# Performance work log

Hardware: AMD Instinct MI355X
Metric: run time of the kernel (lower is better)

Reference implementation:

```python
import jax, jax.numpy as jnp
import numpy as np


def _ln(x, g, eps=1e-5):
    # channel LayerNorm over dim 1, unbiased=False variance
    mean = jnp.mean(x, axis=1, keepdims=True)
    var = jnp.mean((x - mean) ** 2, axis=1, keepdims=True)
    return (x - mean) * jax.lax.rsqrt(var + eps) * g


def _c11(x, w, b):
    # 1x1 conv: w (O,C), b (O,)
    return jnp.einsum('bchw,oc->bohw', x, w) + b[None, :, None, None]


def _dw(x, w, b):
    # depthwise 3x3 conv, SAME padding; w (C,1,3,3), b (C,)
    C = x.shape[1]
    y = jax.lax.conv_general_dilated(x, w, (1, 1), 'SAME',
                                     feature_group_count=C,
                                     dimension_numbers=('NCHW', 'OIHW', 'NCHW'))
    return y + b[None, :, None, None]


def _forward(F_i, F_w, g1, g2, qw1, qb1, kw1, kb1, vw1, vb1,
             qw2, qb2, kw2, kb2, vw2, vb2,
             qdw1, qdb1, kdw1, kdb1, vdw1, vdb1,
             qdw2, qdb2, kdw2, kdb2, vdw2, vdb2, lw, lb):
    B, C1, H, W = F_i.shape
    C2 = F_w.shape[1]
    HW = H * W
    fi = _ln(F_i, g1)
    fw = _ln(F_w, g2)
    # qkv = 1x1 conv -> depthwise conv; then RAW C-order reshape (torch .view)
    Qi = _dw(_c11(fi, qw1, qb1), qdw1, qdb1).reshape(B, HW, C1)
    Ki = _dw(_c11(fi, kw1, kb1), kdw1, kdb1).reshape(B, HW, C1)
    Vi = _dw(_c11(fi, vw1, vb1), vdw1, vdb1).reshape(B, C1, HW)
    Qw = _dw(_c11(fw, qw2, qb2), qdw2, qdb2).reshape(B, HW, C2)
    Kw = _dw(_c11(fw, kw2, kb2), kdw2, kdb2).reshape(B, HW, C2)
    Vw = _dw(_c11(fw, vw2, vb2), vdw2, vdb2).reshape(B, C2, HW)
    # channel cross-attention: (B,C1,HW)@(B,HW,C2) -> (B,C1,C2)
    a1 = jax.nn.softmax(jnp.einsum('bnc,bnd->bcd', Qi, Kw), axis=-1)
    a2 = jax.nn.softmax(jnp.einsum('bnc,bnd->bcd', Qw, Ki), axis=-1)
    Aw = jnp.einsum('bcd,bdn->bcn', a1, Vw).reshape(B, H, W, C2).transpose(0, 3, 1, 2)
    Ai = jnp.einsum('bcd,bdn->bcn', a2, Vi).reshape(B, H, W, C1).transpose(0, 3, 1, 2)
    cat = jnp.concatenate([Aw, Ai], axis=1)  # (B, C2+C1, H, W)
    Ct = cat.shape[1]
    flat = cat.reshape(B, Ct, HW).transpose(0, 2, 1).reshape(-1, Ct)  # (B*HW, Ct)
    out = flat @ lw.T + lb  # (B*HW, Cout)
    Cout = lb.shape[0]
    # faithful replication of torch's view/permute/view tail
    out = out.reshape(B, Cout, H, W).transpose(0, 2, 3, 1).reshape(B, Cout, H, W)
    return out + F_i + F_w


def setup_inputs() -> dict:
    key = jax.random.key(0)
    ks = jax.random.split(key, 20)
    B, C, H, W = 8, 128, 128, 128
    d = {}
    d['F_i'] = jax.random.normal(ks[0], (B, C, H, W), jnp.float32)
    d['F_w'] = jax.random.normal(ks[1], (B, C, H, W), jnp.float32)
    d['g1'] = jnp.ones((1, C, 1, 1), jnp.float32)
    d['g2'] = jnp.ones((1, C, 1, 1), jnp.float32)
    s = 1.0 / np.sqrt(C)
    i = 2
    for n in ['qw1', 'kw1', 'vw1', 'qw2', 'kw2', 'vw2']:
        d[n] = jax.random.normal(ks[i], (C, C), jnp.float32) * s
        i += 1
    for n in ['qb1', 'kb1', 'vb1', 'qb2', 'kb2', 'vb2']:
        d[n] = jnp.zeros((C,), jnp.float32)
    sd = 1.0 / 3.0
    for n in ['qdw1', 'kdw1', 'vdw1', 'qdw2', 'kdw2', 'vdw2']:
        d[n] = jax.random.normal(ks[i], (C, 1, 3, 3), jnp.float32) * sd
        i += 1
    for n in ['qdb1', 'kdb1', 'vdb1', 'qdb2', 'kdb2', 'vdb2']:
        d[n] = jnp.zeros((C,), jnp.float32)
    d['lw'] = jax.random.normal(ks[i], (C, 2 * C), jnp.float32) * (1.0 / np.sqrt(2 * C))
    d['lb'] = jnp.zeros((C,), jnp.float32)
    return d


def reference(F_i, F_w, g1, g2, qw1, qb1, kw1, kb1, vw1, vb1,
              qw2, qb2, kw2, kb2, vw2, vb2,
              qdw1, qdb1, kdw1, kdb1, vdw1, vdb1,
              qdw2, qdb2, kdw2, kdb2, vdw2, vdb2, lw, lb):
    return _forward(F_i, F_w, g1, g2, qw1, qb1, kw1, kb1, vw1, vb1,
                    qw2, qb2, kw2, kb2, vw2, vb2,
                    qdw1, qdb1, kdw1, kdb1, vdw1, vdb1,
                    qdw2, qdb2, kdw2, kdb2, vdw2, vdb2, lw, lb)
```

## Files before the change

### kernel.cpp

```cpp
#include <hip/hip_runtime.h>
#include <cstddef>
#include <cstring>

#define HW 16384
#define CC 128
#define NB 8
#define GB 4

typedef short bf16x8_t __attribute__((ext_vector_type(8)));
typedef float floatx4 __attribute__((ext_vector_type(4)));

__device__ inline unsigned short f2bf(float f) {
  unsigned u; __builtin_memcpy(&u, &f, 4);
  u += 0x7fffu + ((u >> 16) & 1u);
  return (unsigned short)(u >> 16);
}
__device__ inline float bf2f(unsigned short s) {
  unsigned u = ((unsigned)s) << 16; float f; __builtin_memcpy(&f, &u, 4);
  return f;
}

__global__ __launch_bounds__(256) void k_ln_stats(const float* __restrict__ x,
                                                  float* __restrict__ mean,
                                                  float* __restrict__ rstd) {
  int idx = blockIdx.x * 256 + threadIdx.x;
  int b = idx >> 14;
  int p = idx & (HW - 1);
  const float* xp = x + ((size_t)b << 21) + p;
  float s = 0.f, ss = 0.f;
  for (int c = 0; c < CC; ++c) {
    float v = xp[(size_t)c << 14];
    s += v;
    ss += v * v;
  }
  float m = s * (1.0f / CC);
  float var = ss * (1.0f / CC) - m * m;
  mean[idx] = m;
  rstd[idx] = rsqrtf(var + 1e-5f);
}

__global__ __launch_bounds__(256) void k_conv1x1_mfma(
    const float* __restrict__ X, const float* __restrict__ W,
    const float* __restrict__ bias, const float* __restrict__ g,
    const float* __restrict__ mean, const float* __restrict__ rstd,
    float* __restrict__ Y, int b0) {
  __shared__ __align__(16) float raw[32][132];
  __shared__ __align__(16) short Ah[128][40];
  __shared__ __align__(16) short Al[128][40];
  __shared__ __align__(16) short Bh[128][40];
  __shared__ __align__(16) short Bl[128][40];
  const int bl = blockIdx.y;
  const int b = b0 + bl;
  const int p0 = blockIdx.x * 128;
  const int t = threadIdx.x;
  const int lane = t & 63, wv = t >> 6;
  const int quad = lane >> 4, l15 = lane & 15;
  const int wr = wv >> 1, wc = wv & 1;

  const int s1c = t >> 3, s1p = (t & 7) * 16;
  const int sao = t >> 1, sas = (t & 1) * 16;
  const int s2p = t & 127, s2o = t >> 7;
  const float mu = mean[b * HW + p0 + s2p];
  const float rs = rstd[b * HW + p0 + s2p];

  const float* Xb = X + ((size_t)b << 21);
  floatx4 acc[4][4];
#pragma unroll
  for (int i = 0; i < 4; ++i)
#pragma unroll
    for (int j = 0; j < 4; ++j) acc[i][j] = (floatx4){0.f, 0.f, 0.f, 0.f};

  for (int k0 = 0; k0 < 128; k0 += 32) {
    {
      const float* xp = Xb + ((size_t)(k0 + s1c) << 14) + p0 + s1p;
#pragma unroll
      for (int u = 0; u < 4; ++u)
        *reinterpret_cast<float4*>(&raw[s1c][s1p + 4 * u]) =
            *reinterpret_cast<const float4*>(xp + 4 * u);
    }
    {
      const float* wp = W + sao * 128 + k0 + sas;
      const float* gp = g + k0 + sas;
      short th[16], tl[16];
#pragma unroll
      for (int j = 0; j < 16; ++j) {
        float v = wp[j] * gp[j];
        unsigned short h = f2bf(v);
        th[j] = (short)h;
        tl[j] = (short)f2bf(v - bf2f(h));
      }
#pragma unroll
      for (int j = 0; j < 2; ++j) {
        *reinterpret_cast<bf16x8_t*>(&Ah[sao][sas + 8 * j]) =
            *reinterpret_cast<bf16x8_t*>(&th[8 * j]);
        *reinterpret_cast<bf16x8_t*>(&Al[sao][sas + 8 * j]) =
            *reinterpret_cast<bf16x8_t*>(&tl[8 * j]);
      }
    }
    __syncthreads();
#pragma unroll
    for (int item = 0; item < 2; ++item) {
      const int oct = s2o + 2 * item;
      short th[8], tl[8];
#pragma unroll
      for (int jj = 0; jj < 8; ++jj) {
        float v = (raw[oct * 8 + jj][s2p] - mu) * rs;
        unsigned short h = f2bf(v);
        th[jj] = (short)h;
        tl[jj] = (short)f2bf(v - bf2f(h));
      }
      *reinterpret_cast<bf16x8_t*>(&Bh[s2p][oct * 8]) =
          *reinterpret_cast<bf16x8_t*>(&th[0]);
      *reinterpret_cast<bf16x8_t*>(&Bl[s2p][oct * 8]) =
          *reinterpret_cast<bf16x8_t*>(&tl[0]);
    }
    __syncthreads();
    bf16x8_t afh[4], afl[4], bfh[4], bfl[4];
#pragma unroll
    for (int i = 0; i < 4; ++i) {
      const int m = wr * 64 + i * 16 + l15;
      afh[i] = *reinterpret_cast<const bf16x8_t*>(&Ah[m][quad * 8]);
      afl[i] = *reinterpret_cast<const bf16x8_t*>(&Al[m][quad * 8]);
    }
#pragma unroll
    for (int j = 0; j < 4; ++j) {
      const int p = wc * 64 + j * 16 + l15;
      bfh[j] = *reinterpret_cast<const bf16x8_t*>(&Bh[p][quad * 8]);
      bfl[j] = *reinterpret_cast<const bf16x8_t*>(&Bl[p][quad * 8]);
    }
#pragma unroll
    for (int i = 0; i < 4; ++i)
#pragma unroll
      for (int j = 0; j < 4; ++j) {
        acc[i][j] = __builtin_amdgcn_mfma_f32_16x16x32_bf16(afh[i], bfh[j], acc[i][j], 0, 0, 0);
        acc[i][j] = __builtin_amdgcn_mfma_f32_16x16x32_bf16(afh[i], bfl[j], acc[i][j], 0, 0, 0);
        acc[i][j] = __builtin_amdgcn_mfma_f32_16x16x32_bf16(afl[i], bfh[j], acc[i][j], 0, 0, 0);
      }
    __syncthreads();
  }
  float* Yb = Y + ((size_t)bl << 21);
#pragma unroll
  for (int i = 0; i < 4; ++i) {
#pragma unroll
    for (int j = 0; j < 4; ++j) {
#pragma unroll
      for (int r = 0; r < 4; ++r) {
        const int o = wr * 64 + i * 16 + quad * 4 + r;
        const int p = p0 + wc * 64 + j * 16 + l15;
        Yb[((size_t)o << 14) + p] = acc[i][j][r] + bias[o];
      }
    }
  }
}

__global__ __launch_bounds__(256) void k_score_dw(
    const float* __restrict__ Yq, const float* __restrict__ Yk,
    const float* __restrict__ qdw, const float* __restrict__ qdb,
    const float* __restrict__ kdw, const float* __restrict__ kdb,
    float* __restrict__ P) {
  __shared__ __align__(16) float As[32][132];
  __shared__ __align__(16) float Bs[32][132];
  const int ch = blockIdx.x;
  const int bl = blockIdx.y;
  const int t = threadIdx.x;
  const int m0 = (t >> 4) * 8, n0 = (t & 15) * 8;
  const int h_loc = t >> 3;
  const int w0 = (t & 7) * 16;
  float acc[8][8];
#pragma unroll
  for (int i = 0; i < 8; ++i)
#pragma unroll
    for (int j = 0; j < 8; ++j) acc[i][j] = 0.f;
  const float* Yqb = Yq + ((size_t)bl << 21);
  const float* Ykb = Yk + ((size_t)bl << 21);
  const int cc = ch;

  for (int k0 = 0; k0 < 128; k0 += 32) {
    const int h = k0 + h_loc;
#pragma unroll
    for (int side = 0; side < 2; ++side) {
      const float* Yc = (side ? Ykb : Yqb) + ((size_t)cc << 14);
      const float* wt = (side ? kdw : qdw) + cc * 9;
      const float bias = (side ? kdb : qdb)[cc];
      float a[16];
#pragma unroll
      for (int j = 0; j < 16; ++j) a[j] = bias;
#pragma unroll
      for (int dy = 0; dy < 3; ++dy) {
        const int hh = h + dy - 1;
        if (hh < 0 || hh > 127) continue;
        const float* rp = Yc + (hh << 7) + w0;
        float4 f0 = *reinterpret_cast<const float4*>(rp);
        float4 f1 = *reinterpret_cast<const float4*>(rp + 4);
        float4 f2 = *reinterpret_cast<const float4*>(rp + 8);
        float4 f3 = *reinterpret_cast<const float4*>(rp + 12);
        float s[18];
        s[1] = f0.x;  s[2] = f0.y;  s[3] = f0.z;  s[4] = f0.w;
        s[5] = f1.x;  s[6] = f1.y;  s[7] = f1.z;  s[8] = f1.w;
        s[9] = f2.x;  s[10] = f2.y; s[11] = f2.z; s[12] = f2.w;
        s[13] = f3.x; s[14] = f3.y; s[15] = f3.z; s[16] = f3.w;
        s[0] = (w0 > 0) ? rp[-1] : 0.f;
        s[17] = (w0 < 112) ? rp[16] : 0.f;
        const float wa = wt[dy * 3 + 0], wb = wt[dy * 3 + 1], wc2 = wt[dy * 3 + 2];
#pragma unroll
        for (int j = 0; j < 16; ++j)
          a[j] = fmaf(s[j], wa, fmaf(s[j + 1], wb, fmaf(s[j + 2], wc2, a[j])));
      }
      float* dst = side ? &Bs[h_loc][w0] : &As[h_loc][w0];
#pragma unroll
      for (int j = 0; j < 16; ++j) dst[j] = a[j];
    }
    __syncthreads();
#pragma unroll
    for (int k = 0; k < 32; ++k) {
      const float4* ap = reinterpret_cast<const float4*>(&As[k][m0]);
      const float4* bp = reinterpret_cast<const float4*>(&Bs[k][n0]);
      float4 a0 = ap[0], a1 = ap[1];
      float4 b0v = bp[0], b1v = bp[1];
      float a[8] = {a0.x, a0.y, a0.z, a0.w, a1.x, a1.y, a1.z, a1.w};
      float bb[8] = {b0v.x, b0v.y, b0v.z, b0v.w, b1v.x, b1v.y, b1v.z, b1v.w};
#pragma unroll
      for (int i = 0; i < 8; ++i)
#pragma unroll
        for (int j = 0; j < 8; ++j) acc[i][j] = fmaf(a[i], bb[j], acc[i][j]);
    }
    __syncthreads();
  }
  float* Pp = P + ((size_t)(ch * GB + bl) << 14);
#pragma unroll
  for (int i = 0; i < 8; ++i)
#pragma unroll
    for (int j = 0; j < 8; ++j) Pp[(m0 + i) * 128 + n0 + j] = acc[i][j];
}

__global__ __launch_bounds__(256) void k_score_reduce(const float* __restrict__ P,
                                                      float* __restrict__ S) {
  int idx = blockIdx.x * 256 + threadIdx.x;
  int bl = idx >> 14;
  int rem = idx & 16383;
  float s = 0.f;
  for (int c = 0; c < 128; ++c) s += P[((size_t)(c * GB + bl) << 14) + rem];
  S[idx] = s;
}

__global__ __launch_bounds__(128) void k_softmax(float* __restrict__ S) {
  __shared__ float red[128];
  const int row = blockIdx.x;
  const int t = threadIdx.x;
  float v = S[row * 128 + t];
  red[t] = v;
  __syncthreads();
  for (int s = 64; s > 0; s >>= 1) {
    if (t < s) red[t] = fmaxf(red[t], red[t + s]);
    __syncthreads();
  }
  float mx = red[0];
  __syncthreads();
  float e = expf(v - mx);
  red[t] = e;
  __syncthreads();
  for (int s = 64; s > 0; s >>= 1) {
    if (t < s) red[t] += red[t + s];
    __syncthreads();
  }
  S[row * 128 + t] = e / red[0];
}

__global__ __launch_bounds__(256) void k_dw_t(const float* __restrict__ Y,
                                              const float* __restrict__ Kw,
                                              const float* __restrict__ db,
                                              unsigned short* __restrict__ Vt) {
  __shared__ unsigned short T[128][33];
  const int h = blockIdx.x;
  const int c0 = blockIdx.y * 32;
  const int bl = blockIdx.z;
  const int t = threadIdx.x;
  const int cl = t >> 3;
  const int w0 = (t & 7) * 16;
  const int c = c0 + cl;
  const float* Yc = Y + ((size_t)bl << 21) + ((size_t)c << 14);
  const float* wt = Kw + c * 9;
  float a[16];
#pragma unroll
  for (int j = 0; j < 16; ++j) a[j] = db[c];
#pragma unroll
  for (int dy = 0; dy < 3; ++dy) {
    const int hh = h + dy - 1;
    if (hh < 0 || hh > 127) continue;
    const float* rp = Yc + (hh << 7) + w0;
    float4 f0 = *reinterpret_cast<const float4*>(rp);
    float4 f1 = *reinterpret_cast<const float4*>(rp + 4);
    float4 f2 = *reinterpret_cast<const float4*>(rp + 8);
    float4 f3 = *reinterpret_cast<const float4*>(rp + 12);
    float s[18];
    s[1] = f0.x;  s[2] = f0.y;  s[3] = f0.z;  s[4] = f0.w;
    s[5] = f1.x;  s[6] = f1.y;  s[7] = f1.z;  s[8] = f1.w;
    s[9] = f2.x;  s[10] = f2.y; s[11] = f2.z; s[12] = f2.w;
    s[13] = f3.x; s[14] = f3.y; s[15] = f3.z; s[16] = f3.w;
    s[0] = (w0 > 0) ? rp[-1] : 0.f;
    s[17] = (w0 < 112) ? rp[16] : 0.f;
    const float wa = wt[dy * 3 + 0], wb = wt[dy * 3 + 1], wc2 = wt[dy * 3 + 2];
#pragma unroll
    for (int j = 0; j < 16; ++j)
      a[j] = fmaf(s[j], wa, fmaf(s[j + 1], wb, fmaf(s[j + 2], wc2, a[j])));
  }
#pragma unroll
  for (int j = 0; j < 16; ++j) T[w0 + j][cl] = f2bf(a[j]);
  __syncthreads();
  const int w = t >> 1, half = t & 1;
  unsigned short tmp[16];
#pragma unroll
  for (int j = 0; j < 16; ++j) tmp[j] = T[w][half * 16 + j];
  uint4 v0, v1;
  unsigned* vp0 = reinterpret_cast<unsigned*>(&v0);
  unsigned* vp1 = reinterpret_cast<unsigned*>(&v1);
#pragma unroll
  for (int j = 0; j < 4; ++j) {
    vp0[j] = (unsigned)tmp[2 * j] | ((unsigned)tmp[2 * j + 1] << 16);
    vp1[j] = (unsigned)tmp[8 + 2 * j] | ((unsigned)tmp[8 + 2 * j + 1] << 16);
  }
  unsigned short* dst = Vt + ((size_t)bl << 21) + ((size_t)((h << 7) + w) << 7)
                        + c0 + half * 16;
  *reinterpret_cast<uint4*>(dst) = v0;
  *reinterpret_cast<uint4*>(dst + 8) = v1;
}

__global__ __launch_bounds__(256) void k_av_mfma(
    const float* __restrict__ S, const unsigned short* __restrict__ Vt,
    unsigned short* __restrict__ O) {
  __shared__ __align__(16) short As[128][136];
  const int bl = blockIdx.y;
  const int p0 = blockIdx.x * 128;
  const int t = threadIdx.x;
  const int lane = t & 63, wv = t >> 6;
  const int quad = lane >> 4, l15 = lane & 15;
  const int wr = wv >> 1, wc = wv & 1;
  {
    const float* Ab = S + ((size_t)bl << 14);
    const int r = t >> 1, hf = (t & 1) * 64;
    const float* src = Ab + r * 128 + hf;
    short tmp[64];
#pragma unroll
    for (int j = 0; j < 64; ++j) tmp[j] = (short)f2bf(src[j]);
#pragma unroll
    for (int j = 0; j < 8; ++j)
      *reinterpret_cast<bf16x8_t*>(&As[r][hf + j * 8]) =
          *reinterpret_cast<bf16x8_t*>(&tmp[j * 8]);
  }
  __syncthreads();
  floatx4 acc[4][4];
#pragma unroll
  for (int i = 0; i < 4; ++i)
#pragma unroll
    for (int j = 0; j < 4; ++j) acc[i][j] = (floatx4){0.f, 0.f, 0.f, 0.f};
  const unsigned short* Vb = Vt + ((size_t)bl << 21);
#pragma unroll
  for (int d0 = 0; d0 < 128; d0 += 32) {
    bf16x8_t af[4], bf[4];
#pragma unroll
    for (int i = 0; i < 4; ++i) {
      const int m = wr * 64 + i * 16 + l15;
      af[i] = *reinterpret_cast<const bf16x8_t*>(&As[m][d0 + quad * 8]);
    }
#pragma unroll
    for (int j = 0; j < 4; ++j) {
      const int p = p0 + wc * 64 + j * 16 + l15;
      bf[j] = *reinterpret_cast<const bf16x8_t*>(Vb + ((size_t)p << 7) + d0 + quad * 8);
    }
#pragma unroll
    for (int i = 0; i < 4; ++i)
#pragma unroll
      for (int j = 0; j < 4; ++j)
        acc[i][j] = __builtin_amdgcn_mfma_f32_16x16x32_bf16(af[i], bf[j], acc[i][j], 0, 0, 0);
  }
  unsigned short* Ob = O + ((size_t)bl << 21);
#pragma unroll
  for (int i = 0; i < 4; ++i) {
#pragma unroll
    for (int j = 0; j < 4; ++j) {
#pragma unroll
      for (int r = 0; r < 4; ++r) {
        const int c = wr * 64 + i * 16 + quad * 4 + r;
        const int p = p0 + wc * 64 + j * 16 + l15;
        Ob[((size_t)c << 14) + p] = f2bf(acc[i][j][r]);
      }
    }
  }
}

__global__ __launch_bounds__(256) void k_final_mfma(
    const unsigned short* __restrict__ Abuf, const float* __restrict__ lw,
    const float* __restrict__ lb, const float* __restrict__ Fi,
    const float* __restrict__ Fw, float* __restrict__ out, int pass, int b0) {
  __shared__ __align__(16) short As[128][136];
  const int c2 = blockIdx.x;
  const int bl = blockIdx.y;
  const int b = b0 + bl;
  const int t = threadIdx.x;
  const int lane = t & 63, wv = t >> 6;
  const int quad = lane >> 4, l15 = lane & 15;
  const int wr = wv >> 1, wc = wv & 1;
  const int koff = pass * 128;
  {
    const int r = t >> 1, hf = (t & 1) * 64;
    const float* src = lw + r * 256 + koff + hf;
    short tmp[64];
#pragma unroll
    for (int j = 0; j < 64; ++j) tmp[j] = (short)f2bf(src[j]);
#pragma unroll
    for (int j = 0; j < 8; ++j)
      *reinterpret_cast<bf16x8_t*>(&As[r][hf + j * 8]) =
          *reinterpret_cast<bf16x8_t*>(&tmp[j * 8]);
  }
  __syncthreads();
  floatx4 acc[4][4];
#pragma unroll
  for (int i = 0; i < 4; ++i)
#pragma unroll
    for (int j = 0; j < 4; ++j) acc[i][j] = (floatx4){0.f, 0.f, 0.f, 0.f};
  const unsigned short* Ub = Abuf + ((size_t)bl << 21) + c2 * 128;
#pragma unroll
  for (int d0 = 0; d0 < 128; d0 += 32) {
    bf16x8_t af[4], bf[4];
#pragma unroll
    for (int i = 0; i < 4; ++i) {
      const int m = wr * 64 + i * 16 + l15;
      af[i] = *reinterpret_cast<const bf16x8_t*>(&As[m][d0 + quad * 8]);
    }
#pragma unroll
    for (int j = 0; j < 4; ++j) {
      const int n = wc * 64 + j * 16 + l15;
      bf[j] = *reinterpret_cast<const bf16x8_t*>(Ub + ((size_t)n << 14) + d0 + quad * 8);
    }
#pragma unroll
    for (int i = 0; i < 4; ++i)
#pragma unroll
      for (int j = 0; j < 4; ++j)
        acc[i][j] = __builtin_amdgcn_mfma_f32_16x16x32_bf16(af[i], bf[j], acc[i][j], 0, 0, 0);
  }
  const size_t obase = ((size_t)b << 21) + ((size_t)c2 << 14);
#pragma unroll
  for (int i = 0; i < 4; ++i) {
#pragma unroll
    for (int j = 0; j < 4; ++j) {
#pragma unroll
      for (int r = 0; r < 4; ++r) {
        const int h2 = wr * 64 + i * 16 + quad * 4 + r;
        const int w2 = wc * 64 + j * 16 + l15;
        const size_t a = obase + ((size_t)h2 << 7) + w2;
        if (pass == 0)
          out[a] = acc[i][j][r] + lb[h2] + Fi[a] + Fw[a];
        else
          out[a] += acc[i][j][r];
      }
    }
  }
}

extern "C" void kernel_launch(void* const* d_in, const int* in_sizes, int n_in,
                              void* d_out, int out_size, void* d_ws, size_t ws_size,
                              hipStream_t stream) {
  const float* F_i  = (const float*)d_in[0];
  const float* F_w  = (const float*)d_in[1];
  const float* g1   = (const float*)d_in[2];
  const float* g2   = (const float*)d_in[3];
  const float* qw1  = (const float*)d_in[4];
  const float* kw1  = (const float*)d_in[5];
  const float* vw1  = (const float*)d_in[6];
  const float* qw2  = (const float*)d_in[7];
  const float* kw2  = (const float*)d_in[8];
  const float* vw2  = (const float*)d_in[9];
  const float* qb1  = (const float*)d_in[10];
  const float* kb1  = (const float*)d_in[11];
  const float* vb1  = (const float*)d_in[12];
  const float* qb2  = (const float*)d_in[13];
  const float* kb2  = (const float*)d_in[14];
  const float* vb2  = (const float*)d_in[15];
  const float* qdw1 = (const float*)d_in[16];
  const float* kdw1 = (const float*)d_in[17];
  const float* vdw1 = (const float*)d_in[18];
  const float* qdw2 = (const float*)d_in[19];
  const float* kdw2 = (const float*)d_in[20];
  const float* vdw2 = (const float*)d_in[21];
  const float* qdb1 = (const float*)d_in[22];
  const float* kdb1 = (const float*)d_in[23];
  const float* vdb1 = (const float*)d_in[24];
  const float* qdb2 = (const float*)d_in[25];
  const float* kdb2 = (const float*)d_in[26];
  const float* vdb2 = (const float*)d_in[27];
  const float* lw   = (const float*)d_in[28];
  const float* lb   = (const float*)d_in[29];
  float* out = (float*)d_out;

  char* w = (char*)d_ws;
  const size_t NTOT = (size_t)NB * HW;
  float* meanI = (float*)w; w += NTOT * 4;
  float* rstdI = (float*)w; w += NTOT * 4;
  float* meanW = (float*)w; w += NTOT * 4;
  float* rstdW = (float*)w; w += NTOT * 4;
  float* S     = (float*)w; w += (size_t)GB * HW * 4;
  float* P     = (float*)w; w += (size_t)128 * GB * HW * 4;
  float* Yq    = (float*)w; w += ((size_t)GB << 21) * 4;
  char*  Ykreg = w;         w += ((size_t)GB << 21) * 4;
  float* Yk    = (float*)Ykreg;
  unsigned short* Vt   = (unsigned short*)Ykreg;
  unsigned short* Abuf = (unsigned short*)(Ykreg + ((size_t)GB << 21) * 2);

  dim3 blk(256);
  k_ln_stats<<<dim3(512), blk, 0, stream>>>(F_i, meanI, rstdI);
  k_ln_stats<<<dim3(512), blk, 0, stream>>>(F_w, meanW, rstdW);

  for (int b0 = 0; b0 < NB; b0 += GB) {
    k_conv1x1_mfma<<<dim3(128, GB), blk, 0, stream>>>(F_i, qw1, qb1, g1, meanI, rstdI, Yq, b0);
    k_conv1x1_mfma<<<dim3(128, GB), blk, 0, stream>>>(F_w, kw2, kb2, g2, meanW, rstdW, Yk, b0);
    k_score_dw<<<dim3(128, GB), blk, 0, stream>>>(Yq, Yk, qdw1, qdb1, kdw2, kdb2, P);
    k_score_reduce<<<dim3(GB * HW / 256), blk, 0, stream>>>(P, S);
    k_softmax<<<dim3(GB * 128), dim3(128), 0, stream>>>(S);
    k_conv1x1_mfma<<<dim3(128, GB), blk, 0, stream>>>(F_w, vw2, vb2, g2, meanW, rstdW, Yq, b0);
    k_dw_t<<<dim3(128, 4, GB), blk, 0, stream>>>(Yq, vdw2, vdb2, Vt);
    k_av_mfma<<<dim3(128, GB), blk, 0, stream>>>(S, Vt, Abuf);
    k_final_mfma<<<dim3(128, GB), blk, 0, stream>>>(Abuf, lw, lb, F_i, F_w, out, 0, b0);

    k_conv1x1_mfma<<<dim3(128, GB), blk, 0, stream>>>(F_w, qw2, qb2, g2, meanW, rstdW, Yq, b0);
    k_conv1x1_mfma<<<dim3(128, GB), blk, 0, stream>>>(F_i, kw1, kb1, g1, meanI, rstdI, Yk, b0);
    k_score_dw<<<dim3(128, GB), blk, 0, stream>>>(Yq, Yk, qdw2, qdb2, kdw1, kdb1, P);
    k_score_reduce<<<dim3(GB * HW / 256), blk, 0, stream>>>(P, S);
    k_softmax<<<dim3(GB * 128), dim3(128), 0, stream>>>(S);
    k_conv1x1_mfma<<<dim3(128, GB), blk, 0, stream>>>(F_i, vw1, vb1, g1, meanI, rstdI, Yq, b0);
    k_dw_t<<<dim3(128, 4, GB), blk, 0, stream>>>(Yq, vdw1, vdb1, Vt);
    k_av_mfma<<<dim3(128, GB), blk, 0, stream>>>(S, Vt, Abuf);
    k_final_mfma<<<dim3(128, GB), blk, 0, stream>>>(Abuf, lw, lb, F_i, F_w, out, 1, b0);
  }
}
```

Measured before the change: 922.0 us.

## Move score GEMM to split-bf16 MFMA and fuse both final projections

The per-channel score kernel now stages the depthwise-conv output in shared memory. It splits each value into a bf16 high and low pair and accumulates with three bf16 MFMAs per tile, replacing the scalar fp32 FMA outer product. Accuracy stays close to fp32 while the multiply work moves onto the matrix cores, at the cost of extra shared memory, extra syncs and conversion work. Separately, the two final-projection launches are merged into one kernel that reads both attention buffers. This removes the read-modify-write of the output and one extra pass over F_i and F_w. It needs a separate workspace buffer for A1.

```diff
diff --git a/kernel.cpp b/kernel.cpp
--- a/kernel.cpp
+++ b/kernel.cpp
@@ -153,35 +153,45 @@
   }
 }
 
-__global__ __launch_bounds__(256) void k_score_dw(
+__global__ __launch_bounds__(256) void k_score_mfma(
     const float* __restrict__ Yq, const float* __restrict__ Yk,
     const float* __restrict__ qdw, const float* __restrict__ qdb,
     const float* __restrict__ kdw, const float* __restrict__ kdb,
     float* __restrict__ P) {
-  __shared__ __align__(16) float As[32][132];
-  __shared__ __align__(16) float Bs[32][132];
+  __shared__ __align__(16) float raw[32][132];
+  __shared__ __align__(16) short Ah[128][40];
+  __shared__ __align__(16) short Al[128][40];
+  __shared__ __align__(16) short Bh[128][40];
+  __shared__ __align__(16) short Bl[128][40];
   const int ch = blockIdx.x;
   const int bl = blockIdx.y;
   const int t = threadIdx.x;
-  const int m0 = (t >> 4) * 8, n0 = (t & 15) * 8;
+  const int lane = t & 63, wv = t >> 6;
+  const int quad = lane >> 4, l15 = lane & 15;
+  const int wr = wv >> 1, wc = wv & 1;
   const int h_loc = t >> 3;
   const int w0 = (t & 7) * 16;
-  float acc[8][8];
-#pragma unroll
-  for (int i = 0; i < 8; ++i)
-#pragma unroll
-    for (int j = 0; j < 8; ++j) acc[i][j] = 0.f;
-  const float* Yqb = Yq + ((size_t)bl << 21);
-  const float* Ykb = Yk + ((size_t)bl << 21);
+  const int s2w = t & 127, s2o = t >> 7;
   const int cc = ch;
+  const float* Yqb = Yq + ((size_t)bl << 21) + ((size_t)cc << 14);
+  const float* Ykb = Yk + ((size_t)bl << 21) + ((size_t)cc << 14);
+  const float* qwt = qdw + cc * 9;
+  const float* kwt = kdw + cc * 9;
+  const float qbv = qdb[cc], kbv = kdb[cc];
+
+  floatx4 acc[4][4];
+#pragma unroll
+  for (int i = 0; i < 4; ++i)
+#pragma unroll
+    for (int j = 0; j < 4; ++j) acc[i][j] = (floatx4){0.f, 0.f, 0.f, 0.f};
 
   for (int k0 = 0; k0 < 128; k0 += 32) {
     const int h = k0 + h_loc;
 #pragma unroll
     for (int side = 0; side < 2; ++side) {
-      const float* Yc = (side ? Ykb : Yqb) + ((size_t)cc << 14);
-      const float* wt = (side ? kdw : qdw) + cc * 9;
-      const float bias = (side ? kdb : qdb)[cc];
+      const float* Yc = side ? Ykb : Yqb;
+      const float* wt = side ? kwt : qwt;
+      const float bias = side ? kbv : qbv;
       float a[16];
 #pragma unroll
       for (int j = 0; j < 16; ++j) a[j] = bias;
@@ -206,31 +216,66 @@
         for (int j = 0; j < 16; ++j)
           a[j] = fmaf(s[j], wa, fmaf(s[j + 1], wb, fmaf(s[j + 2], wc2, a[j])));
       }
-      float* dst = side ? &Bs[h_loc][w0] : &As[h_loc][w0];
-#pragma unroll
-      for (int j = 0; j < 16; ++j) dst[j] = a[j];
-    }
-    __syncthreads();
-#pragma unroll
-    for (int k = 0; k < 32; ++k) {
-      const float4* ap = reinterpret_cast<const float4*>(&As[k][m0]);
-      const float4* bp = reinterpret_cast<const float4*>(&Bs[k][n0]);
-      float4 a0 = ap[0], a1 = ap[1];
-      float4 b0v = bp[0], b1v = bp[1];
-      float a[8] = {a0.x, a0.y, a0.z, a0.w, a1.x, a1.y, a1.z, a1.w};
-      float bb[8] = {b0v.x, b0v.y, b0v.z, b0v.w, b1v.x, b1v.y, b1v.z, b1v.w};
-#pragma unroll
-      for (int i = 0; i < 8; ++i)
-#pragma unroll
-        for (int j = 0; j < 8; ++j) acc[i][j] = fmaf(a[i], bb[j], acc[i][j]);
-    }
-    __syncthreads();
+#pragma unroll
+      for (int u = 0; u < 4; ++u)
+        *reinterpret_cast<float4*>(&raw[h_loc][w0 + 4 * u]) =
+            (float4){a[4 * u], a[4 * u + 1], a[4 * u + 2], a[4 * u + 3]};
+      __syncthreads();
+      short* dh = side ? &Bh[0][0] : &Ah[0][0];
+      short* dl = side ? &Bl[0][0] : &Al[0][0];
+#pragma unroll
+      for (int item = 0; item < 2; ++item) {
+        const int oct = s2o + 2 * item;
+        short th[8], tl[8];
+#pragma unroll
+        for (int jj = 0; jj < 8; ++jj) {
+          float v = raw[oct * 8 + jj][s2w];
+          unsigned short hb = f2bf(v);
+          th[jj] = (short)hb;
+          tl[jj] = (short)f2bf(v - bf2f(hb));
+        }
+        *reinterpret_cast<bf16x8_t*>(&dh[s2w * 40 + oct * 8]) =
+            *reinterpret_cast<bf16x8_t*>(&th[0]);
+        *reinterpret_cast<bf16x8_t*>(&dl[s2w * 40 + oct * 8]) =
+            *reinterpret_cast<bf16x8_t*>(&tl[0]);
+      }
+      __syncthreads();
+    }
+    bf16x8_t afh[4], afl[4], bfh[4], bfl[4];
+#pragma unroll
+    for (int i = 0; i < 4; ++i) {
+      const int m = wr * 64 + i * 16 + l15;
+      afh[i] = *reinterpret_cast<const bf16x8_t*>(&Ah[m][quad * 8]);
+      afl[i] = *reinterpret_cast<const bf16x8_t*>(&Al[m][quad * 8]);
+    }
+#pragma unroll
+    for (int j = 0; j < 4; ++j) {
+      const int n = wc * 64 + j * 16 + l15;
+      bfh[j] = *reinterpret_cast<const bf16x8_t*>(&Bh[n][quad * 8]);
+      bfl[j] = *reinterpret_cast<const bf16x8_t*>(&Bl[n][quad * 8]);
+    }
+#pragma unroll
+    for (int i = 0; i < 4; ++i)
+#pragma unroll
+      for (int j = 0; j < 4; ++j) {
+        acc[i][j] = __builtin_amdgcn_mfma_f32_16x16x32_bf16(afh[i], bfh[j], acc[i][j], 0, 0, 0);
+        acc[i][j] = __builtin_amdgcn_mfma_f32_16x16x32_bf16(afh[i], bfl[j], acc[i][j], 0, 0, 0);
+        acc[i][j] = __builtin_amdgcn_mfma_f32_16x16x32_bf16(afl[i], bfh[j], acc[i][j], 0, 0, 0);
+      }
   }
   float* Pp = P + ((size_t)(ch * GB + bl) << 14);
 #pragma unroll
-  for (int i = 0; i < 8; ++i)
-#pragma unroll
-    for (int j = 0; j < 8; ++j) Pp[(m0 + i) * 128 + n0 + j] = acc[i][j];
+  for (int i = 0; i < 4; ++i) {
+#pragma unroll
+    for (int j = 0; j < 4; ++j) {
+#pragma unroll
+      for (int r = 0; r < 4; ++r) {
+        const int c = wr * 64 + i * 16 + quad * 4 + r;
+        const int d = wc * 64 + j * 16 + l15;
+        Pp[c * 128 + d] = acc[i][j][r];
+      }
+    }
+  }
 }
 
 __global__ __launch_bounds__(256) void k_score_reduce(const float* __restrict__ P,
@@ -388,10 +433,11 @@
   }
 }
 
-__global__ __launch_bounds__(256) void k_final_mfma(
-    const unsigned short* __restrict__ Abuf, const float* __restrict__ lw,
-    const float* __restrict__ lb, const float* __restrict__ Fi,
-    const float* __restrict__ Fw, float* __restrict__ out, int pass, int b0) {
+__global__ __launch_bounds__(256) void k_final2_mfma(
+    const unsigned short* __restrict__ A1, const unsigned short* __restrict__ A2,
+    const float* __restrict__ lw, const float* __restrict__ lb,
+    const float* __restrict__ Fi, const float* __restrict__ Fw,
+    float* __restrict__ out, int b0) {
   __shared__ __align__(16) short As[128][136];
   const int c2 = blockIdx.x;
   const int bl = blockIdx.y;
@@ -400,43 +446,46 @@
   const int lane = t & 63, wv = t >> 6;
   const int quad = lane >> 4, l15 = lane & 15;
   const int wr = wv >> 1, wc = wv & 1;
-  const int koff = pass * 128;
-  {
-    const int r = t >> 1, hf = (t & 1) * 64;
-    const float* src = lw + r * 256 + koff + hf;
-    short tmp[64];
-#pragma unroll
-    for (int j = 0; j < 64; ++j) tmp[j] = (short)f2bf(src[j]);
-#pragma unroll
-    for (int j = 0; j < 8; ++j)
-      *reinterpret_cast<bf16x8_t*>(&As[r][hf + j * 8]) =
-          *reinterpret_cast<bf16x8_t*>(&tmp[j * 8]);
-  }
-  __syncthreads();
   floatx4 acc[4][4];
 #pragma unroll
   for (int i = 0; i < 4; ++i)
 #pragma unroll
     for (int j = 0; j < 4; ++j) acc[i][j] = (floatx4){0.f, 0.f, 0.f, 0.f};
-  const unsigned short* Ub = Abuf + ((size_t)bl << 21) + c2 * 128;
-#pragma unroll
-  for (int d0 = 0; d0 < 128; d0 += 32) {
-    bf16x8_t af[4], bf[4];
-#pragma unroll
-    for (int i = 0; i < 4; ++i) {
-      const int m = wr * 64 + i * 16 + l15;
-      af[i] = *reinterpret_cast<const bf16x8_t*>(&As[m][d0 + quad * 8]);
-    }
-#pragma unroll
-    for (int j = 0; j < 4; ++j) {
-      const int n = wc * 64 + j * 16 + l15;
-      bf[j] = *reinterpret_cast<const bf16x8_t*>(Ub + ((size_t)n << 14) + d0 + quad * 8);
-    }
-#pragma unroll
-    for (int i = 0; i < 4; ++i)
-#pragma unroll
-      for (int j = 0; j < 4; ++j)
-        acc[i][j] = __builtin_amdgcn_mfma_f32_16x16x32_bf16(af[i], bf[j], acc[i][j], 0, 0, 0);
+#pragma unroll
+  for (int phase = 0; phase < 2; ++phase) {
+    {
+      const int r = t >> 1, hf = (t & 1) * 64;
+      const float* src = lw + r * 256 + phase * 128 + hf;
+      short tmp[64];
+#pragma unroll
+      for (int j = 0; j < 64; ++j) tmp[j] = (short)f2bf(src[j]);
+#pragma unroll
+      for (int j = 0; j < 8; ++j)
+        *reinterpret_cast<bf16x8_t*>(&As[r][hf + j * 8]) =
+            *reinterpret_cast<bf16x8_t*>(&tmp[j * 8]);
+    }
+    __syncthreads();
+    const unsigned short* Ub = (phase ? A2 : A1) + ((size_t)bl << 21) + c2 * 128;
+#pragma unroll
+    for (int d0 = 0; d0 < 128; d0 += 32) {
+      bf16x8_t af[4], bf[4];
+#pragma unroll
+      for (int i = 0; i < 4; ++i) {
+        const int m = wr * 64 + i * 16 + l15;
+        af[i] = *reinterpret_cast<const bf16x8_t*>(&As[m][d0 + quad * 8]);
+      }
+#pragma unroll
+      for (int j = 0; j < 4; ++j) {
+        const int n = wc * 64 + j * 16 + l15;
+        bf[j] = *reinterpret_cast<const bf16x8_t*>(Ub + ((size_t)n << 14) + d0 + quad * 8);
+      }
+#pragma unroll
+      for (int i = 0; i < 4; ++i)
+#pragma unroll
+        for (int j = 0; j < 4; ++j)
+          acc[i][j] = __builtin_amdgcn_mfma_f32_16x16x32_bf16(af[i], bf[j], acc[i][j], 0, 0, 0);
+    }
+    __syncthreads();
   }
   const size_t obase = ((size_t)b << 21) + ((size_t)c2 << 14);
 #pragma unroll
@@ -448,10 +497,7 @@
         const int h2 = wr * 64 + i * 16 + quad * 4 + r;
         const int w2 = wc * 64 + j * 16 + l15;
         const size_t a = obase + ((size_t)h2 << 7) + w2;
-        if (pass == 0)
-          out[a] = acc[i][j][r] + lb[h2] + Fi[a] + Fw[a];
-        else
-          out[a] += acc[i][j][r];
+        out[a] = acc[i][j][r] + lb[h2] + Fi[a] + Fw[a];
       }
     }
   }
@@ -503,8 +549,9 @@
   float* Yq    = (float*)w; w += ((size_t)GB << 21) * 4;
   char*  Ykreg = w;         w += ((size_t)GB << 21) * 4;
   float* Yk    = (float*)Ykreg;
-  unsigned short* Vt   = (unsigned short*)Ykreg;
-  unsigned short* Abuf = (unsigned short*)(Ykreg + ((size_t)GB << 21) * 2);
+  unsigned short* Vt = (unsigned short*)Ykreg;
+  unsigned short* A2 = (unsigned short*)(Ykreg + ((size_t)GB << 21) * 2);
+  unsigned short* A1 = (unsigned short*)w; w += ((size_t)GB << 21) * 2;
 
   dim3 blk(256);
   k_ln_stats<<<dim3(512), blk, 0, stream>>>(F_i, meanI, rstdI);
@@ -513,22 +560,22 @@
   for (int b0 = 0; b0 < NB; b0 += GB) {
     k_conv1x1_mfma<<<dim3(128, GB), blk, 0, stream>>>(F_i, qw1, qb1, g1, meanI, rstdI, Yq, b0);
     k_conv1x1_mfma<<<dim3(128, GB), blk, 0, stream>>>(F_w, kw2, kb2, g2, meanW, rstdW, Yk, b0);
-    k_score_dw<<<dim3(128, GB), blk, 0, stream>>>(Yq, Yk, qdw1, qdb1, kdw2, kdb2, P);
+    k_score_mfma<<<dim3(128, GB), blk, 0, stream>>>(Yq, Yk, qdw1, qdb1, kdw2, kdb2, P);
     k_score_reduce<<<dim3(GB * HW / 256), blk, 0, stream>>>(P, S);
     k_softmax<<<dim3(GB * 128), dim3(128), 0, stream>>>(S);
     k_conv1x1_mfma<<<dim3(128, GB), blk, 0, stream>>>(F_w, vw2, vb2, g2, meanW, rstdW, Yq, b0);
     k_dw_t<<<dim3(128, 4, GB), blk, 0, stream>>>(Yq, vdw2, vdb2, Vt);
-    k_av_mfma<<<dim3(128, GB), blk, 0, stream>>>(S, Vt, Abuf);
-    k_final_mfma<<<dim3(128, GB), blk, 0, stream>>>(Abuf, lw, lb, F_i, F_w, out, 0, b0);
+    k_av_mfma<<<dim3(128, GB), blk, 0, stream>>>(S, Vt, A1);
 
     k_conv1x1_mfma<<<dim3(128, GB), blk, 0, stream>>>(F_w, qw2, qb2, g2, meanW, rstdW, Yq, b0);
     k_conv1x1_mfma<<<dim3(128, GB), blk, 0, stream>>>(F_i, kw1, kb1, g1, meanI, rstdI, Yk, b0);
-    k_score_dw<<<dim3(128, GB), blk, 0, stream>>>(Yq, Yk, qdw2, qdb2, kdw1, kdb1, P);
+    k_score_mfma<<<dim3(128, GB), blk, 0, stream>>>(Yq, Yk, qdw2, qdb2, kdw1, kdb1, P);
     k_score_reduce<<<dim3(GB * HW / 256), blk, 0, stream>>>(P, S);
     k_softmax<<<dim3(GB * 128), dim3(128), 0, stream>>>(S);
     k_conv1x1_mfma<<<dim3(128, GB), blk, 0, stream>>>(F_i, vw1, vb1, g1, meanI, rstdI, Yq, b0);
     k_dw_t<<<dim3(128, 4, GB), blk, 0, stream>>>(Yq, vdw1, vdb1, Vt);
-    k_av_mfma<<<dim3(128, GB), blk, 0, stream>>>(S, Vt, Abuf);
-    k_final_mfma<<<dim3(128, GB), blk, 0, stream>>>(Abuf, lw, lb, F_i, F_w, out, 1, b0);
-  }
-}
+    k_av_mfma<<<dim3(128, GB), blk, 0, stream>>>(S, Vt, A2);
+
+    k_final2_mfma<<<dim3(128, GB), blk, 0, stream>>>(A1, A2, lw, lb, F_i, F_w, out, b0);
+  }
+}
```

After: 838.9 us. 9.0% less time.
